# Kernel optimization log

Hardware: AMD Instinct MI355X
Metric: run time of the kernel (lower is better)

The kernel has to match this reference:

```python
import jax, jax.numpy as jnp
import numpy as np

ATT_WIDTH = 64  # local attention width, history_only=False
MASK_PENALTY = 10000.0


def setup_inputs() -> dict:
    key = jax.random.key(0)
    ks = jax.random.split(key, 4)
    B, L, D, U = 2, 1024, 256, 64
    x = jax.random.normal(ks[0], (B, L, D), dtype=jnp.float32)
    Wt = jax.random.normal(ks[1], (D, U), dtype=jnp.float32) * (1.0 / np.sqrt(D))
    Wx = jax.random.normal(ks[2], (D, U), dtype=jnp.float32) * (1.0 / np.sqrt(D))
    bh = jnp.zeros((U,), dtype=jnp.float32)
    Wa = jax.random.normal(ks[3], (U, 1), dtype=jnp.float32) * (1.0 / np.sqrt(U))
    ba = jnp.zeros((1,), dtype=jnp.float32)
    return {"x": x, "Wt": Wt, "Wx": Wx, "bh": bh, "Wa": Wa, "ba": ba}


def reference(x, Wt, Wx, bh, Wa, ba):
    B, L, D = x.shape
    # additive emission: e[b,i,j] = tanh(x_i Wt + x_j Wx + bh) . wa + ba
    q = jnp.einsum('bld,du->blu', x, Wt)  # [B,L,U]
    k = jnp.einsum('bld,du->blu', x, Wx)  # [B,L,U]
    h = jnp.tanh(q[:, :, None, :] + k[:, None, :, :] + bh)  # [B,L,L,U]
    e = jnp.einsum('biju,u->bij', h, Wa[:, 0]) + ba[0]  # [B,L,L]
    # local-width band mask (history_only=False -> centered window)
    idx = jnp.arange(L)
    lower = idx - ATT_WIDTH // 2          # [L]
    upper = lower + ATT_WIDTH             # [L]
    band = (lower[:, None] <= idx[None, :]) & (idx[None, :] < upper[:, None])
    e = e - MASK_PENALTY * (1.0 - band.astype(e.dtype))
    a = jax.nn.softmax(e, axis=-1)        # [B,L,L]
    v = jnp.einsum('bij,bjd->bid', a, x)  # [B,L,D]
    return v
```

## Files before the change

kernel.cpp:

```cpp
#include <hip/hip_runtime.h>


#define NROWS 2048
#define LSEQ  1024
#define DDIM  256
#define UDIM  64

__global__ __launch_bounds__(256) void qk_kernel(
    const float* __restrict__ x, const float* __restrict__ Wt,
    const float* __restrict__ Wx, const float* __restrict__ bh,
    float* __restrict__ q, float* __restrict__ kT) {
  int t   = threadIdx.x;
  int u   = t & 63;
  int sel = (t >> 6) & 1;
  int row = blockIdx.x * 2 + (t >> 7);
  const float* __restrict__ W = sel ? Wx : Wt;
  const float4* __restrict__ xr = (const float4*)(x + row * DDIM);
  float acc = 0.f;
#pragma unroll 8
  for (int d4 = 0; d4 < DDIM / 4; ++d4) {
    float4 xv = xr[d4];
    const float* wp = W + d4 * 4 * UDIM + u;
    acc += xv.x * wp[0] + xv.y * wp[64] + xv.z * wp[128] + xv.w * wp[192];
  }
  if (sel == 0) q[row * UDIM + u] = acc + bh[u];
  else          kT[u * NROWS + row] = acc;
}

__device__ __forceinline__ float tanh_fast(float v) {
  float t = __expf(-2.f * v);
  return 2.f * __builtin_amdgcn_rcpf(1.f + t) - 1.f;
}

__global__ __launch_bounds__(256) void attn_kernel(
    const float* __restrict__ x, const float* __restrict__ q,
    const float* __restrict__ kT, const float* __restrict__ Wa,
    float* __restrict__ out) {
  int lane = threadIdx.x & 63;
  int wid  = threadIdx.x >> 6;
  int grow = blockIdx.x * 4 + wid;
  int b = grow >> 10;
  int i = grow & (LSEQ - 1);
  int lo = max(0, i - 32);
  int hi = min(LSEQ, i + 32);

  __shared__ float qs[4][UDIM];
  __shared__ float was[UDIM];
  qs[wid][lane] = q[grow * UDIM + lane];
  if (threadIdx.x < UDIM) was[threadIdx.x] = Wa[threadIdx.x];
  __syncthreads();

  int  j     = lo + lane;
  bool valid = j < hi;
  int  jc    = valid ? j : hi - 1;
  const float* __restrict__ kp = kT + b * LSEQ + jc;
  float e = 0.f;
#pragma unroll 8
  for (int u = 0; u < UDIM; ++u) {
    float kv = kp[u * NROWS];
    e += was[u] * tanh_fast(qs[wid][u] + kv);
  }

  float m = valid ? e : -3.4e38f;
#pragma unroll
  for (int off = 32; off >= 1; off >>= 1) m = fmaxf(m, __shfl_xor(m, off));
  float p = valid ? __expf(e - m) : 0.f;
  float s = p;
#pragma unroll
  for (int off = 32; off >= 1; off >>= 1) s += __shfl_xor(s, off);
  float a = p * __builtin_amdgcn_rcpf(s);

  const float4* __restrict__ xb = (const float4*)(x + (b * LSEQ + lo) * DDIM);
  float4 acc = make_float4(0.f, 0.f, 0.f, 0.f);
  int wlen = hi - lo;
  if (wlen == 64) {
#pragma unroll 8
    for (int jj = 0; jj < 64; ++jj) {
      float aj = __shfl(a, jj);
      float4 xv = xb[jj * 64 + lane];
      acc.x += aj * xv.x; acc.y += aj * xv.y; acc.z += aj * xv.z; acc.w += aj * xv.w;
    }
  } else {
    for (int jj = 0; jj < wlen; ++jj) {
      float aj = __shfl(a, jj);
      float4 xv = xb[jj * 64 + lane];
      acc.x += aj * xv.x; acc.y += aj * xv.y; acc.z += aj * xv.z; acc.w += aj * xv.w;
    }
  }
  float4* o4 = (float4*)(out + grow * DDIM);
  o4[lane] = acc;
}

extern "C" void kernel_launch(void* const* d_in, const int* in_sizes, int n_in,
                              void* d_out, int out_size, void* d_ws, size_t ws_size,
                              hipStream_t stream) {
  const float* x  = (const float*)d_in[0];
  const float* Wt = (const float*)d_in[1];
  const float* Wx = (const float*)d_in[2];
  const float* bh = (const float*)d_in[3];
  const float* Wa = (const float*)d_in[4];
  float* out = (float*)d_out;

  float* q  = (float*)d_ws;
  float* kT = q + NROWS * UDIM;

  qk_kernel<<<NROWS / 2, 256, 0, stream>>>(x, Wt, Wx, bh, q, kT);
  attn_kernel<<<NROWS / 4, 256, 0, stream>>>(x, q, kT, Wa, out);
}
```

Measured before the change: 98.77 us.

## Share K window and x rows across four query rows per block via LDS

```diff
diff --git a/kernel.cpp b/kernel.cpp
--- a/kernel.cpp
+++ b/kernel.cpp
@@ -1,30 +1,43 @@
 #include <hip/hip_runtime.h>
 
 
-#define NROWS 2048
 #define LSEQ  1024
 #define DDIM  256
 #define UDIM  64
+#define NROWS 2048
+#define RPB   4
+#define JMAX  68
 
 __global__ __launch_bounds__(256) void qk_kernel(
     const float* __restrict__ x, const float* __restrict__ Wt,
     const float* __restrict__ Wx, const float* __restrict__ bh,
-    float* __restrict__ q, float* __restrict__ kT) {
-  int t   = threadIdx.x;
-  int u   = t & 63;
+    float* __restrict__ q, float* __restrict__ k) {
+  int t = threadIdx.x;
+  int u = t & 63;
   int sel = (t >> 6) & 1;
-  int row = blockIdx.x * 2 + (t >> 7);
+  int r0 = blockIdx.x * 8 + (t >> 7) * 4;
   const float* __restrict__ W = sel ? Wx : Wt;
-  const float4* __restrict__ xr = (const float4*)(x + row * DDIM);
-  float acc = 0.f;
-#pragma unroll 8
+  const float4* __restrict__ x0 = (const float4*)(x + (r0 + 0) * DDIM);
+  const float4* __restrict__ x1 = (const float4*)(x + (r0 + 1) * DDIM);
+  const float4* __restrict__ x2 = (const float4*)(x + (r0 + 2) * DDIM);
+  const float4* __restrict__ x3 = (const float4*)(x + (r0 + 3) * DDIM);
+  float a0 = 0.f, a1 = 0.f, a2 = 0.f, a3 = 0.f;
+#pragma unroll 4
   for (int d4 = 0; d4 < DDIM / 4; ++d4) {
-    float4 xv = xr[d4];
     const float* wp = W + d4 * 4 * UDIM + u;
-    acc += xv.x * wp[0] + xv.y * wp[64] + xv.z * wp[128] + xv.w * wp[192];
+    float w0 = wp[0], w1 = wp[64], w2 = wp[128], w3 = wp[192];
+    float4 v0 = x0[d4], v1 = x1[d4], v2 = x2[d4], v3 = x3[d4];
+    a0 += v0.x * w0 + v0.y * w1 + v0.z * w2 + v0.w * w3;
+    a1 += v1.x * w0 + v1.y * w1 + v1.z * w2 + v1.w * w3;
+    a2 += v2.x * w0 + v2.y * w1 + v2.z * w2 + v2.w * w3;
+    a3 += v3.x * w0 + v3.y * w1 + v3.z * w2 + v3.w * w3;
   }
-  if (sel == 0) q[row * UDIM + u] = acc + bh[u];
-  else          kT[u * NROWS + row] = acc;
+  float* __restrict__ dst = sel ? k : q;
+  float bias = sel ? 0.f : bh[u];
+  dst[(r0 + 0) * UDIM + u] = a0 + bias;
+  dst[(r0 + 1) * UDIM + u] = a1 + bias;
+  dst[(r0 + 2) * UDIM + u] = a2 + bias;
+  dst[(r0 + 3) * UDIM + u] = a3 + bias;
 }
 
 __device__ __forceinline__ float tanh_fast(float v) {
@@ -32,63 +45,79 @@
   return 2.f * __builtin_amdgcn_rcpf(1.f + t) - 1.f;
 }
 
+__device__ __forceinline__ float bcast(float v, int l) {
+  return __uint_as_float(__builtin_amdgcn_readlane(__float_as_uint(v), l));
+}
+
 __global__ __launch_bounds__(256) void attn_kernel(
     const float* __restrict__ x, const float* __restrict__ q,
-    const float* __restrict__ kT, const float* __restrict__ Wa,
+    const float* __restrict__ k, const float* __restrict__ Wa,
     float* __restrict__ out) {
-  int lane = threadIdx.x & 63;
-  int wid  = threadIdx.x >> 6;
-  int grow = blockIdx.x * 4 + wid;
-  int b = grow >> 10;
-  int i = grow & (LSEQ - 1);
+  __shared__ float k_lds[JMAX][UDIM + 1];
+  __shared__ float a_lds[RPB][JMAX];
+
+  int t = threadIdx.x;
+  int lane = t & 63;
+  int wid = t >> 6;
+  int g0 = blockIdx.x * RPB;
+  int b = g0 >> 10;
+  int i0 = g0 & (LSEQ - 1);
+  int jbase = max(0, i0 - 32);
+  int jend = min(LSEQ, i0 + RPB - 1 + 32);
+  int jcount = jend - jbase;
+
+  for (int jj = wid; jj < jcount; jj += 4)
+    k_lds[jj][lane] = k[(b * LSEQ + jbase + jj) * UDIM + lane];
+  for (int z = t; z < RPB * JMAX; z += 256) ((float*)a_lds)[z] = 0.f;
+  float qv = q[(g0 + wid) * UDIM + lane];
+  float wv = Wa[lane];
+  __syncthreads();
+
+  int i = i0 + wid;
   int lo = max(0, i - 32);
   int hi = min(LSEQ, i + 32);
-
-  __shared__ float qs[4][UDIM];
-  __shared__ float was[UDIM];
-  qs[wid][lane] = q[grow * UDIM + lane];
-  if (threadIdx.x < UDIM) was[threadIdx.x] = Wa[threadIdx.x];
-  __syncthreads();
-
-  int  j     = lo + lane;
-  bool valid = j < hi;
-  int  jc    = valid ? j : hi - 1;
-  const float* __restrict__ kp = kT + b * LSEQ + jc;
+  int off = lo - jbase;
+  bool valid = (lo + lane) < hi;
+  const float* __restrict__ kr = &k_lds[off + lane][0];
   float e = 0.f;
-#pragma unroll 8
-  for (int u = 0; u < UDIM; ++u) {
-    float kv = kp[u * NROWS];
-    e += was[u] * tanh_fast(qs[wid][u] + kv);
-  }
+#pragma unroll
+  for (int u = 0; u < UDIM; ++u)
+    e += bcast(wv, u) * tanh_fast(bcast(qv, u) + kr[u]);
 
   float m = valid ? e : -3.4e38f;
 #pragma unroll
-  for (int off = 32; off >= 1; off >>= 1) m = fmaxf(m, __shfl_xor(m, off));
+  for (int o = 32; o >= 1; o >>= 1) m = fmaxf(m, __shfl_xor(m, o));
   float p = valid ? __expf(e - m) : 0.f;
   float s = p;
 #pragma unroll
-  for (int off = 32; off >= 1; off >>= 1) s += __shfl_xor(s, off);
-  float a = p * __builtin_amdgcn_rcpf(s);
+  for (int o = 32; o >= 1; o >>= 1) s += __shfl_xor(s, o);
+  a_lds[wid][off + lane] = p * __builtin_amdgcn_rcpf(s);
+  __syncthreads();
 
-  const float4* __restrict__ xb = (const float4*)(x + (b * LSEQ + lo) * DDIM);
-  float4 acc = make_float4(0.f, 0.f, 0.f, 0.f);
-  int wlen = hi - lo;
-  if (wlen == 64) {
-#pragma unroll 8
-    for (int jj = 0; jj < 64; ++jj) {
-      float aj = __shfl(a, jj);
-      float4 xv = xb[jj * 64 + lane];
-      acc.x += aj * xv.x; acc.y += aj * xv.y; acc.z += aj * xv.z; acc.w += aj * xv.w;
-    }
-  } else {
-    for (int jj = 0; jj < wlen; ++jj) {
-      float aj = __shfl(a, jj);
-      float4 xv = xb[jj * 64 + lane];
-      acc.x += aj * xv.x; acc.y += aj * xv.y; acc.z += aj * xv.z; acc.w += aj * xv.w;
-    }
+  const float* __restrict__ xq = x + b * LSEQ * DDIM + wid * 64 + lane;
+  float c0 = 0.f, c1 = 0.f, c2 = 0.f, c3 = 0.f;
+  int nch = (jcount + 3) >> 2;
+  for (int ch = 0; ch < nch; ++ch) {
+    int jj = ch * 4;
+    float4 A0 = *(const float4*)&a_lds[0][jj];
+    float4 A1 = *(const float4*)&a_lds[1][jj];
+    float4 A2 = *(const float4*)&a_lds[2][jj];
+    float4 A3 = *(const float4*)&a_lds[3][jj];
+    int j0 = jbase + jj;
+    float xv0 = xq[min(j0 + 0, jend - 1) * DDIM];
+    float xv1 = xq[min(j0 + 1, jend - 1) * DDIM];
+    float xv2 = xq[min(j0 + 2, jend - 1) * DDIM];
+    float xv3 = xq[min(j0 + 3, jend - 1) * DDIM];
+    c0 += A0.x * xv0 + A0.y * xv1 + A0.z * xv2 + A0.w * xv3;
+    c1 += A1.x * xv0 + A1.y * xv1 + A1.z * xv2 + A1.w * xv3;
+    c2 += A2.x * xv0 + A2.y * xv1 + A2.z * xv2 + A2.w * xv3;
+    c3 += A3.x * xv0 + A3.y * xv1 + A3.z * xv2 + A3.w * xv3;
   }
-  float4* o4 = (float4*)(out + grow * DDIM);
-  o4[lane] = acc;
+  float* __restrict__ ob = out + g0 * DDIM + wid * 64 + lane;
+  ob[0 * DDIM] = c0;
+  ob[1 * DDIM] = c1;
+  ob[2 * DDIM] = c2;
+  ob[3 * DDIM] = c3;
 }
 
 extern "C" void kernel_launch(void* const* d_in, const int* in_sizes, int n_in,
@@ -101,9 +130,9 @@
   const float* Wa = (const float*)d_in[4];
   float* out = (float*)d_out;
 
-  float* q  = (float*)d_ws;
-  float* kT = q + NROWS * UDIM;
+  float* q = (float*)d_ws;
+  float* k = q + NROWS * UDIM;
 
-  qk_kernel<<<NROWS / 2, 256, 0, stream>>>(x, Wt, Wx, bh, q, kT);
-  attn_kernel<<<NROWS / 4, 256, 0, stream>>>(x, q, kT, Wa, out);
+  qk_kernel<<<NROWS / 8, 256, 0, stream>>>(x, Wt, Wx, bh, q, k);
+  attn_kernel<<<NROWS / RPB, 256, 0, stream>>>(x, q, k, Wa, out);
 }
```

After: 90.83 us. -8.0%, faster.
